# Kernel tuning notes

Measured on AMD Instinct MI355X. Metric: run time of the kernel, lower is better.

## Reference

```python
import jax, jax.numpy as jnp
import numpy as np

HEADS, OUT_C = 8, 16
NEG_SLOPE = 0.2  # PyG GATConv default negative_slope


def setup_inputs() -> dict:
    key = jax.random.key(0)
    ks = jax.random.split(key, 6)
    N, E, IN = 100000, 1600000, 128
    x = jax.random.normal(ks[0], (N, IN), jnp.float32)
    edge_index = jax.random.randint(ks[1], (2, E), 0, N, dtype=jnp.int32)
    W = jax.random.normal(ks[2], (IN, HEADS * OUT_C), jnp.float32) / np.float32(np.sqrt(IN))
    att_src = jax.random.normal(ks[3], (HEADS, OUT_C), jnp.float32) * 0.1
    att_dst = jax.random.normal(ks[4], (HEADS, OUT_C), jnp.float32) * 0.1
    bias = jax.random.normal(ks[5], (HEADS * OUT_C,), jnp.float32) * 0.01
    return {"x": x, "edge_index": edge_index, "W": W,
            "att_src": att_src, "att_dst": att_dst, "bias": bias}


def reference(x, edge_index, W, att_src, att_dst, bias):
    N = x.shape[0]
    # Linear projection, split into heads: [N, H, C]
    xw = (x @ W).reshape(N, HEADS, OUT_C)
    # Add self-loops (PyG default add_self_loops=True)
    loops = jnp.arange(N, dtype=edge_index.dtype)
    src = jnp.concatenate([edge_index[0], loops])
    dst = jnp.concatenate([edge_index[1], loops])
    # Per-node attention terms [N, H], then per-edge logits
    a_s = jnp.einsum('nhc,hc->nh', xw, att_src)
    a_d = jnp.einsum('nhc,hc->nh', xw, att_dst)
    e = a_s[src] + a_d[dst]                       # [Etot, H]
    e = jnp.where(e > 0, e, NEG_SLOPE * e)        # LeakyReLU
    # Segment softmax over edges grouped by destination node
    emax = jax.ops.segment_max(e, dst, num_segments=N)
    p = jnp.exp(e - emax[dst])
    denom = jax.ops.segment_sum(p, dst, num_segments=N)
    alpha = p / (denom[dst] + 1e-16)              # [Etot, H]
    # Weighted scatter-aggregate of source messages
    out = jax.ops.segment_sum(xw[src] * alpha[:, :, None], dst, num_segments=N)
    out = out.reshape(N, HEADS * OUT_C) + bias    # concat heads + bias
    return jax.nn.relu(out)                       # act='relu', norm=None
```

## Files before the change

kernel.cpp:

```cpp
#include <hip/hip_runtime.h>
#include <math.h>

#define HEADS 8
#define OUTC 16
#define HC 128
#define NEG_SLOPE 0.2f

#define BM 128
#define BK 16
#define XPAD 132
#define CAP 64

typedef unsigned int uint;
typedef unsigned short ushort;

__device__ __forceinline__ ushort f2bf(float f) {
    uint u = __float_as_uint(f);
    u += 0x7FFFu + ((u >> 16) & 1u);
    return (ushort)(u >> 16);
}

__global__ __launch_bounds__(256, 4) void k_fused(
    const float* __restrict__ x, const float* __restrict__ W,
    const float* __restrict__ att_src, const float* __restrict__ att_dst,
    const int* __restrict__ ei,
    ushort* __restrict__ xwh, float* __restrict__ a_s, float* __restrict__ a_d,
    int* __restrict__ deg, int* __restrict__ csr,
    int N, int E, int GB) {
    __shared__ float xs[BK][XPAD];
    __shared__ float Ws[BK][XPAD];

    if (blockIdx.x >= GB) {
        int e = (blockIdx.x - GB) * 256 + threadIdx.x;
        if (e < E) {
            int src = ei[e];
            int dst = ei[E + e];
            int slot = atomicAdd(&deg[dst], 1);
            if (slot < CAP) csr[(size_t)dst * CAP + slot] = src;
        }
        return;
    }

    int t = threadIdx.x;
    int nb0 = blockIdx.x * BM;
    int tc = t & 15;
    int tr = t >> 4;

    float acc[8][8];
#pragma unroll
    for (int i = 0; i < 8; ++i)
#pragma unroll
        for (int j = 0; j < 8; ++j) acc[i][j] = 0.0f;

    for (int k0 = 0; k0 < HC; k0 += BK) {
        int kk4 = (t & 3) * 4;
#pragma unroll
        for (int p = 0; p < 2; ++p) {
            int nr = (t >> 2) + p * 64;
            int node = nb0 + nr;
            float4 v = make_float4(0.f, 0.f, 0.f, 0.f);
            if (node < N) v = *(const float4*)&x[(size_t)node * HC + k0 + kk4];
            xs[kk4 + 0][nr] = v.x;
            xs[kk4 + 1][nr] = v.y;
            xs[kk4 + 2][nr] = v.z;
            xs[kk4 + 3][nr] = v.w;
        }
        int kk = t >> 4;
        int c4 = (t & 15) * 4;
        *(float4*)&Ws[kk][c4] = *(const float4*)&W[(size_t)(k0 + kk) * HC + c4];
        *(float4*)&Ws[kk][c4 + 64] =
            *(const float4*)&W[(size_t)(k0 + kk) * HC + c4 + 64];
        __syncthreads();

#pragma unroll 4
        for (int k = 0; k < BK; ++k) {
            float xa[8], wa[8];
            *(float4*)&xa[0] = *(const float4*)&xs[k][tr * 8];
            *(float4*)&xa[4] = *(const float4*)&xs[k][tr * 8 + 4];
            *(float4*)&wa[0] = *(const float4*)&Ws[k][tc * 4];
            *(float4*)&wa[4] = *(const float4*)&Ws[k][tc * 4 + 64];
#pragma unroll
            for (int i = 0; i < 8; ++i)
#pragma unroll
                for (int j = 0; j < 8; ++j)
                    acc[i][j] = fmaf(xa[i], wa[j], acc[i][j]);
        }
        __syncthreads();
    }

    float as8[8], ad8[8];
#pragma unroll
    for (int j = 0; j < 4; ++j) {
        as8[j] = att_src[tc * 4 + j];
        ad8[j] = att_dst[tc * 4 + j];
        as8[j + 4] = att_src[64 + tc * 4 + j];
        ad8[j + 4] = att_dst[64 + tc * 4 + j];
    }
    int h0 = tc >> 2;
#pragma unroll
    for (int i = 0; i < 8; ++i) {
        int node = nb0 + tr * 8 + i;
        float vs0 = 0.f, vd0 = 0.f, vs1 = 0.f, vd1 = 0.f;
        ushort hlo[4], hhi[4];
#pragma unroll
        for (int j = 0; j < 4; ++j) {
            vs0 = fmaf(acc[i][j], as8[j], vs0);
            vd0 = fmaf(acc[i][j], ad8[j], vd0);
            vs1 = fmaf(acc[i][j + 4], as8[j + 4], vs1);
            vd1 = fmaf(acc[i][j + 4], ad8[j + 4], vd1);
            hlo[j] = f2bf(acc[i][j]);
            hhi[j] = f2bf(acc[i][j + 4]);
        }
        vs0 += __shfl_xor(vs0, 1); vs0 += __shfl_xor(vs0, 2);
        vd0 += __shfl_xor(vd0, 1); vd0 += __shfl_xor(vd0, 2);
        vs1 += __shfl_xor(vs1, 1); vs1 += __shfl_xor(vs1, 2);
        vd1 += __shfl_xor(vd1, 1); vd1 += __shfl_xor(vd1, 2);
        if (node < N) {
            *(uint2*)&xwh[(size_t)node * HC + tc * 4] = *(uint2*)&hlo[0];
            *(uint2*)&xwh[(size_t)node * HC + 64 + tc * 4] = *(uint2*)&hhi[0];
            if ((tc & 3) == 0) {
                a_s[node * HEADS + h0] = vs0;
                a_d[node * HEADS + h0] = vd0;
                a_s[node * HEADS + 4 + h0] = vs1;
                a_d[node * HEADS + 4 + h0] = vd1;
            }
        }
    }
}

__global__ __launch_bounds__(256) void k_node(
    const int* __restrict__ deg, const int* __restrict__ csr,
    const float* __restrict__ a_s, const float* __restrict__ a_d,
    const uint* __restrict__ xwh, const float* __restrict__ bias,
    float* __restrict__ out, int N) {
    int n = blockIdx.x * 4 + (threadIdx.x >> 6);
    if (n >= N) return;
    int l = threadIdx.x & 63;
    int hB = l >> 3;

    float asn = a_s[n * HEADS + hB];
    float adn = a_d[n * HEADS + hB];

    float v = asn + adn;
    v = v > 0.0f ? v : NEG_SLOPE * v;
    float p = __expf(v);
    float den = p;
    uint w = xwh[n * 64 + l];
    float acc0 = p * __uint_as_float(w << 16);
    float acc1 = p * __uint_as_float(w & 0xFFFF0000u);

    int cnt = deg[n];
    if (cnt > CAP) cnt = CAP;
    const int* row = csr + (size_t)n * CAP;
#pragma unroll 8
    for (int i = 0; i < cnt; ++i) {
        int s = row[i];
        float vv = a_s[s * HEADS + hB] + adn;
        vv = vv > 0.0f ? vv : NEG_SLOPE * vv;
        float pp = __expf(vv);
        den += pp;
        uint ww = xwh[s * 64 + l];
        acc0 = fmaf(pp, __uint_as_float(ww << 16), acc0);
        acc1 = fmaf(pp, __uint_as_float(ww & 0xFFFF0000u), acc1);
    }

    float inv = 1.0f / (den + 1e-16f);
    float2 b = *(const float2*)&bias[2 * l];
    float r0 = acc0 * inv + b.x;
    float r1 = acc1 * inv + b.y;
    float2 o;
    o.x = r0 > 0.0f ? r0 : 0.0f;
    o.y = r1 > 0.0f ? r1 : 0.0f;
    *(float2*)&out[(size_t)n * HC + 2 * l] = o;
}

extern "C" void kernel_launch(void* const* d_in, const int* in_sizes, int n_in,
                              void* d_out, int out_size, void* d_ws, size_t ws_size,
                              hipStream_t stream) {
    const float* x       = (const float*)d_in[0];
    const int*   ei      = (const int*)d_in[1];
    const float* W       = (const float*)d_in[2];
    const float* att_src = (const float*)d_in[3];
    const float* att_dst = (const float*)d_in[4];
    const float* bias    = (const float*)d_in[5];
    float* out = (float*)d_out;

    int N = in_sizes[0] / HC;
    int E = in_sizes[1] / 2;

    ushort* xwh = (ushort*)d_ws;
    float* a_s  = (float*)(xwh + (size_t)N * HC);
    float* a_d  = a_s + (size_t)N * HEADS;
    int* deg    = (int*)(a_d + (size_t)N * HEADS);
    int* csr    = deg + N;

    hipMemsetAsync(deg, 0, (size_t)N * sizeof(int), stream);

    int GB = (N + BM - 1) / BM;
    int SB = (E + 255) / 256;
    k_fused<<<GB + SB, 256, 0, stream>>>(x, W, att_src, att_dst, ei,
                                         xwh, a_s, a_d, deg, csr, N, E, GB);

    k_node<<<(N + 3) / 4, 256, 0, stream>>>(deg, csr, a_s, a_d,
                                            (const uint*)xwh, bias, out, N);
}
```

Baseline: 284.7 us.

## Interleave GEMM and scatter blocks, prefetch GEMM tiles into registers

Even-numbered blocks now run the projection GEMM and odd-numbered blocks run the CSR-building edge scatter as a grid-stride loop. This replaces the old layout of all GEMM blocks followed by many small scatter blocks, so the compute-bound and atomic-bound work run on the GPU at the same time. The GEMM K-tile doubles to 32 and register double-buffering is added, loading the next x/W tile from global memory while the current one is computed. The trade-off is higher register and LDS use, which may reduce occupancy, and fewer scatter threads each handling more edges.

```diff
diff --git a/kernel.cpp b/kernel.cpp
--- a/kernel.cpp
+++ b/kernel.cpp
@@ -7,7 +7,7 @@
 #define NEG_SLOPE 0.2f
 
 #define BM 128
-#define BK 16
+#define BK 32
 #define XPAD 132
 #define CAP 64
 
@@ -30,9 +30,11 @@
     __shared__ float xs[BK][XPAD];
     __shared__ float Ws[BK][XPAD];
 
-    if (blockIdx.x >= GB) {
-        int e = (blockIdx.x - GB) * 256 + threadIdx.x;
-        if (e < E) {
+    int t = threadIdx.x;
+
+    if (blockIdx.x & 1) {
+        int stride = GB * 256;
+        for (int e = (blockIdx.x >> 1) * 256 + t; e < E; e += stride) {
             int src = ei[e];
             int dst = ei[E + e];
             int slot = atomicAdd(&deg[dst], 1);
@@ -41,36 +43,59 @@
         return;
     }
 
-    int t = threadIdx.x;
-    int nb0 = blockIdx.x * BM;
+    int nb0 = (blockIdx.x >> 1) * BM;
     int tc = t & 15;
     int tr = t >> 4;
 
+    int kk4 = (t & 7) * 4;
+    int nr0 = t >> 3;
+    int kkW = t >> 3;
+    int c4 = (t & 7) * 4;
+
     float acc[8][8];
 #pragma unroll
     for (int i = 0; i < 8; ++i)
 #pragma unroll
         for (int j = 0; j < 8; ++j) acc[i][j] = 0.0f;
 
-    for (int k0 = 0; k0 < HC; k0 += BK) {
-        int kk4 = (t & 3) * 4;
-#pragma unroll
-        for (int p = 0; p < 2; ++p) {
-            int nr = (t >> 2) + p * 64;
-            int node = nb0 + nr;
-            float4 v = make_float4(0.f, 0.f, 0.f, 0.f);
-            if (node < N) v = *(const float4*)&x[(size_t)node * HC + k0 + kk4];
-            xs[kk4 + 0][nr] = v.x;
-            xs[kk4 + 1][nr] = v.y;
-            xs[kk4 + 2][nr] = v.z;
-            xs[kk4 + 3][nr] = v.w;
-        }
-        int kk = t >> 4;
-        int c4 = (t & 15) * 4;
-        *(float4*)&Ws[kk][c4] = *(const float4*)&W[(size_t)(k0 + kk) * HC + c4];
-        *(float4*)&Ws[kk][c4 + 64] =
-            *(const float4*)&W[(size_t)(k0 + kk) * HC + c4 + 64];
+    float4 xf[4], wf[4];
+#pragma unroll
+    for (int p = 0; p < 4; ++p) {
+        int node = nb0 + nr0 + 32 * p;
+        xf[p] = (node < N) ? *(const float4*)&x[(size_t)node * HC + kk4]
+                           : make_float4(0.f, 0.f, 0.f, 0.f);
+    }
+#pragma unroll
+    for (int j = 0; j < 4; ++j)
+        wf[j] = *(const float4*)&W[(size_t)kkW * HC + c4 + 32 * j];
+
+    for (int t0 = 0; t0 < HC / BK; ++t0) {
+#pragma unroll
+        for (int p = 0; p < 4; ++p) {
+            int nr = nr0 + 32 * p;
+            xs[kk4 + 0][nr] = xf[p].x;
+            xs[kk4 + 1][nr] = xf[p].y;
+            xs[kk4 + 2][nr] = xf[p].z;
+            xs[kk4 + 3][nr] = xf[p].w;
+        }
+#pragma unroll
+        for (int j = 0; j < 4; ++j)
+            *(float4*)&Ws[kkW][c4 + 32 * j] = wf[j];
         __syncthreads();
+
+        if (t0 < HC / BK - 1) {
+            int k0n = (t0 + 1) * BK;
+#pragma unroll
+            for (int p = 0; p < 4; ++p) {
+                int node = nb0 + nr0 + 32 * p;
+                xf[p] = (node < N)
+                            ? *(const float4*)&x[(size_t)node * HC + k0n + kk4]
+                            : make_float4(0.f, 0.f, 0.f, 0.f);
+            }
+#pragma unroll
+            for (int j = 0; j < 4; ++j)
+                wf[j] = *(const float4*)&W[(size_t)(k0n + kkW) * HC + c4 + 32 * j];
+        }
 
 #pragma unroll 4
         for (int k = 0; k < BK; ++k) {
@@ -197,9 +222,8 @@
     hipMemsetAsync(deg, 0, (size_t)N * sizeof(int), stream);
 
     int GB = (N + BM - 1) / BM;
-    int SB = (E + 255) / 256;
-    k_fused<<<GB + SB, 256, 0, stream>>>(x, W, att_src, att_dst, ei,
-                                         xwh, a_s, a_d, deg, csr, N, E, GB);
+    k_fused<<<2 * GB, 256, 0, stream>>>(x, W, att_src, att_dst, ei,
+                                        xwh, a_s, a_d, deg, csr, N, E, GB);
 
     k_node<<<(N + 3) / 4, 256, 0, stream>>>(deg, csr, a_s, a_d,
                                             (const uint*)xwh, bias, out, N);
```

Result: slower. 308.1 us (+8.2%).
